# Optimization experiments

Hardware: AMD Instinct MI355X
Metric: run time of the kernel (lower is better)

## Reference

```python
import math
import jax, jax.numpy as jnp
import numpy as np

B, H, M, L, D, HID = 4, 8, 1024, 3200, 128, 1024
ATTN_LIM, RAMP = 2048, 128
PRE_DIV, LOSS_COEF = 16.0, 1e-06
SIZE = ATTN_LIM  # ExpireSpanDrop size = args.attn_lim


def skew(X, pad_value):
    # X: (BH, M, K) -> (BH, M, K+M), shifting row i right by i (relative-pos trick)
    BH, Mq, K = X.shape
    X = jnp.pad(X, ((0, 0), (0, 0), (0, Mq + 1)), constant_values=pad_value)
    X = X.reshape(BH, -1)[:, :-Mq]
    return X.reshape(BH, Mq, K + Mq)


def setup_inputs():
    key = jax.random.key(0)
    ks = jax.random.split(key, 6)
    query = jax.random.normal(ks[0], (B * H, M, D), jnp.float32)
    k = jax.random.normal(ks[1], (B * H, L, D), jnp.float32)
    v = jax.random.normal(ks[2], (B * H, L, D), jnp.float32)
    memory_hid = jax.random.normal(ks[3], (B, L, HID), jnp.float32)
    # age counters: oldest slot first; the current block (last M slots) goes down to -(M-1)
    memory_counter = jnp.broadcast_to(
        jnp.arange(L - 1, -1, -1, dtype=jnp.float32) - (M - 1), (B, L))
    key_pe = 0.02 * jax.random.normal(ks[4], (1, D, M), jnp.float32)
    span_w = 0.01 * jax.random.normal(ks[5], (1, HID), jnp.float32)
    span_b = jnp.full((1,), -math.log(1.0 / 0.1 - 1.0), jnp.float32)  # init_percentage=0.1
    return {"query": query, "key": k, "value": v, "memory_hid": memory_hid,
            "memory_counter": memory_counter, "key_pe": key_pe,
            "span_w": span_w, "span_b": span_b}


def reference(query, key, value, memory_hid, memory_counter, key_pe, span_w, span_b):
    max_mem = ATTN_LIM + M + RAMP
    # QK^T
    attn = jnp.einsum('bmd,bld->bml', query, key)                              # (BH, M, L)
    # --- ExpireSpanDrop (eval mode, no noise) ---
    max_span = jax.nn.sigmoid(
        jnp.einsum('blh,oh->blo', memory_hid / PRE_DIV, span_w)[..., 0] + span_b[0]) * SIZE  # (B, L)
    remaining_offset = max_span - memory_counter                               # (B, L)
    remaining_span = remaining_offset[:, None, :] - jnp.arange(M, dtype=jnp.float32)[None, :, None]  # (B, M, L)
    emask = jnp.clip(remaining_span / RAMP + 1.0, 0.0, 1.0)
    ramp_mask = ((emask > 0) & (emask < 1)).astype(emask.dtype)
    aux_loss = (remaining_span * ramp_mask).sum((-1, -2)) / RAMP / M * LOSS_COEF  # (B,)
    # causal mask (precomputed buffer in torch)
    causal = jnp.tril(jnp.ones((M, max_mem), jnp.float32), k=max_mem - M - 1)[:, -L:]
    mask = jnp.broadcast_to((emask * causal)[:, None], (B, H, M, L)).reshape(B * H, M, L)
    # --- relative position bias via skew ---
    attn_pos = skew(jnp.einsum('bmd,dk->bmk', query, key_pe[0]), 0.0)          # (BH, M, 2M)
    attn = attn.at[:, :, -2 * M:].add(attn_pos)
    # masked softmax + renormalization by soft mask
    attn = jnp.where(mask == 0, -jnp.inf, attn) / math.sqrt(D)
    attn = jax.nn.softmax(attn, axis=-1)
    attn = attn * mask
    attn = attn / (attn.sum(-1, keepdims=True) + 1e-08)
    out = jnp.einsum('bml,bld->bmd', attn, value)                              # (BH, M, D)
    return out, aux_loss, remaining_offset
```

## Files before the change

kernel.cpp:

```cpp
#include <hip/hip_runtime.h>
#include <stdint.h>

#define B_   4
#define H_   8
#define BH_  32
#define M_   1024
#define L_   3200
#define D_   128
#define HID_ 1024
#define NT64 50
#define CAUSAL_K 2175
#define POS_OFF  1152
#define SCALE 0.08838834764831845f
#define NEGV (-3.0e38f)
#define NEGH (-1.0e38f)

typedef short  bf16x8 __attribute__((ext_vector_type(8)));
typedef float  f32x4  __attribute__((ext_vector_type(4)));

__device__ __forceinline__ unsigned short f2bf(float x) {
    union { float f; uint32_t u; } v; v.f = x;
    return (unsigned short)((v.u + 0x7FFFu + ((v.u >> 16) & 1u)) >> 16);
}
__device__ __forceinline__ float bf2f(unsigned short h) {
    union { uint32_t u; float f; } v; v.u = ((uint32_t)h) << 16; return v.f;
}
__device__ __forceinline__ uint32_t pack_bf2(float lo, float hi) {
    union { float f; uint32_t u; } a, b; a.f = lo; b.f = hi;
    return __builtin_amdgcn_perm(b.u, a.u, 0x07060302u);
}

template <int CTRL>
__device__ __forceinline__ float dpp_movf(float x) {
    union { float f; int i; } u; u.f = x;
    u.i = __builtin_amdgcn_update_dpp(0, u.i, CTRL, 0xF, 0xF, true);
    return u.f;
}
__device__ __forceinline__ float row_max16(float x) {
    x = fmaxf(x, dpp_movf<0xB1>(x));
    x = fmaxf(x, dpp_movf<0x4E>(x));
    x = fmaxf(x, dpp_movf<0x141>(x));
    x = fmaxf(x, dpp_movf<0x140>(x));
    return x;
}
__device__ __forceinline__ float row_sum16(float x) {
    x += dpp_movf<0xB1>(x);
    x += dpp_movf<0x4E>(x);
    x += dpp_movf<0x141>(x);
    x += dpp_movf<0x140>(x);
    return x;
}

__global__ void span_kernel(const float* __restrict__ hid,
                            const float* __restrict__ counter,
                            const float* __restrict__ sw,
                            const float* __restrict__ sb,
                            float* __restrict__ r0_ws,
                            float* __restrict__ r0_out) {
    const int row  = blockIdx.x * 4 + (threadIdx.x >> 6);
    const int lane = threadIdx.x & 63;
    const float* h = hid + (size_t)row * HID_;
    float acc = 0.f;
#pragma unroll
    for (int it = 0; it < 4; ++it) {
        const int k = it * 256 + lane * 4;
        const float4 a = *(const float4*)(h + k);
        const float4 w = *(const float4*)(sw + k);
        acc += a.x*w.x + a.y*w.y + a.z*w.z + a.w*w.w;
    }
#pragma unroll
    for (int off = 32; off; off >>= 1) acc += __shfl_down(acc, off);
    if (lane == 0) {
        const float x  = acc * (1.0f/16.0f) + sb[0];
        const float ms = 2048.0f / (1.0f + __expf(-x));
        const float r0 = ms - counter[row];
        r0_ws[row]  = r0;
        r0_out[row] = r0;
    }
}

__global__ void tilemax_kernel(const float* __restrict__ r0_ws,
                               float* __restrict__ tmax) {
    const int t = blockIdx.x;
    const int lane = threadIdx.x;
    float v = r0_ws[t * 64 + lane];
#pragma unroll
    for (int off = 32; off; off >>= 1) v = fmaxf(v, __shfl_down(v, off));
    if (lane == 0) tmax[t] = v;
}

__global__ void aux_kernel(const float* __restrict__ r0_ws,
                           float* __restrict__ aux_out) {
    const int b = blockIdx.x, tid = threadIdx.x;
    float s = 0.f;
    for (int l = tid; l < L_; l += 256) {
        const float r = r0_ws[b * L_ + l];
        const int fl = (int)floorf(r);
        int mlo = fl + 1;   if (mlo < 0) mlo = 0;
        int mhi = fl + 128; if (mhi > M_ - 1) mhi = M_ - 1;
        const int n = mhi - mlo + 1;
        if (n > 0) s += (float)n * r - 0.5f * (float)(mlo + mhi) * (float)n;
    }
    __shared__ float red[256];
    red[tid] = s; __syncthreads();
    for (int st = 128; st; st >>= 1) {
        if (tid < st) red[tid] += red[tid + st];
        __syncthreads();
    }
    if (tid == 0) aux_out[b] = red[0] * (1.0f/128.0f) * (1.0f/1024.0f) * 1e-6f;
}

__global__ void pet_kernel(const float* __restrict__ PE,
                           unsigned short* __restrict__ PET) {
    const int tid = threadIdx.x;
    const int c = blockIdx.x * 4 + (tid >> 6);
    const int e = tid & 63;
    const float lo = PE[(2*e)   * M_ + c];
    const float hi = PE[(2*e+1) * M_ + c];
    ((uint32_t*)PET)[c * 64 + e] = pack_bf2(lo, hi);
}

#define KS_STR 136
#define VT_STR 72
#define PE_STR 136
#define P_STR  72
#define T_STR  72

__global__ void __launch_bounds__(256, 2)
attn_kernel(const float* __restrict__ Q, const float* __restrict__ K,
            const float* __restrict__ V, const unsigned short* __restrict__ PET,
            const float* __restrict__ r0g, const float* __restrict__ tmax,
            float* __restrict__ out) {
    __shared__ short Ks[64 * KS_STR];
    __shared__ short Vt[128 * VT_STR];
    __shared__ short PEs[64 * PE_STR];
    __shared__ short Tb[2][64 * T_STR];
    __shared__ short Pb[64 * P_STR];
    __shared__ float r0s[64];
    __shared__ float tfl[NT64];

    const int bh = blockIdx.y;
    const int b  = bh >> 3;
    const int i0 = blockIdx.x << 6;
    const int tid  = threadIdx.x;
    const int wave = tid >> 6;
    const int lane = tid & 63;
    const int lq   = lane & 15;
    const int quad = lane >> 4;
    const int lt_end = min(NT64, (int)blockIdx.x + 35);

    if (tid < NT64) tfl[tid] = tmax[b * NT64 + tid];
    __syncthreads();
    const float live_thresh = (float)(i0 - 128);

    auto next_live = [&](int s) {
        while (s < lt_end && !(tfl[s] > live_thresh)) ++s;
        return s;
    };

    float4 kp[8];
    float4 vpa[4], vpb[4];
    uint4  pep[4];
    float  r0p = 0.f;

    auto issue_prefetch = [&](int plt) {
        const int l0p = plt << 6;
        const float* kb = K + ((size_t)bh * L_ + l0p) * D_;
        const float* vb = V + ((size_t)bh * L_ + l0p) * D_;
#pragma unroll
        for (int it = 0; it < 8; ++it) {
            const int f = it * 256 + tid;
            kp[it] = *(const float4*)(kb + (f >> 5) * D_ + (f & 31) * 4);
        }
        const int p2 = (tid & 31) * 2;
#pragma unroll
        for (int it = 0; it < 4; ++it) {
            const int c = it * 8 + (tid >> 5);
            vpa[it] = *(const float4*)(vb + (size_t)p2 * D_ + c * 4);
            vpb[it] = *(const float4*)(vb + (size_t)(p2 + 1) * D_ + c * 4);
        }
        const int c0p = l0p - i0 - POS_OFF;
#pragma unroll
        for (int it = 0; it < 4; ++it) {
            const int f = it * 256 + tid;
            const int cg = c0p + (f >> 4);
            if ((unsigned)cg < (unsigned)M_)
                pep[it] = *(const uint4*)(PET + (size_t)cg * D_ + (f & 15) * 8);
            else { pep[it].x = 0; pep[it].y = 0; pep[it].z = 0; pep[it].w = 0; }
        }
        if (tid < 64) r0p = r0g[b * L_ + l0p + tid];
    };

    auto write_stage = [&]() {
#pragma unroll
        for (int it = 0; it < 8; ++it) {
            const int f = it * 256 + tid;
            uint2 w;
            w.x = pack_bf2(kp[it].x, kp[it].y);
            w.y = pack_bf2(kp[it].z, kp[it].w);
            *(uint2*)&Ks[(f >> 5) * KS_STR + (f & 31) * 4] = w;
        }
        const int p2 = (tid & 31) * 2;
#pragma unroll
        for (int it = 0; it < 4; ++it) {
            const int c = it * 8 + (tid >> 5);
            const float* a = (const float*)&vpa[it];
            const float* bb = (const float*)&vpb[it];
#pragma unroll
            for (int j = 0; j < 4; ++j)
                *(uint32_t*)&Vt[(c * 4 + j) * VT_STR + p2] = pack_bf2(a[j], bb[j]);
        }
#pragma unroll
        for (int it = 0; it < 4; ++it) {
            const int f = it * 256 + tid;
            *(uint4*)&PEs[(f >> 4) * PE_STR + (f & 15) * 8] = pep[it];
        }
        if (tid < 64) r0s[tid] = r0p;
    };

    int lt = next_live(0);
    if (lt < lt_end) issue_prefetch(lt);

    bf16x8 qfrag[4];
    {
        const float* qp = Q + ((size_t)bh * M_ + (i0 + wave * 16 + lq)) * D_;
#pragma unroll
        for (int kk = 0; kk < 4; ++kk) {
            const float4 q0 = *(const float4*)(qp + kk * 32 + quad * 8);
            const float4 q1 = *(const float4*)(qp + kk * 32 + quad * 8 + 4);
            union { bf16x8 v; uint32_t u[4]; } qq;
            qq.u[0] = pack_bf2(q0.x, q0.y); qq.u[1] = pack_bf2(q0.z, q0.w);
            qq.u[2] = pack_bf2(q1.x, q1.y); qq.u[3] = pack_bf2(q1.z, q1.w);
            qfrag[kk] = qq.v;
        }
    }

    auto computeT = [&](short* tb) {
#pragma unroll
        for (int nt = 0; nt < 4; ++nt) {
            f32x4 acc = (f32x4){0.f, 0.f, 0.f, 0.f};
#pragma unroll
            for (int kk = 0; kk < 4; ++kk) {
                const bf16x8 bf = *(const bf16x8*)&PEs[(nt*16 + lq) * PE_STR + kk*32 + quad*8];
                acc = __builtin_amdgcn_mfma_f32_16x16x32_bf16(qfrag[kk], bf, acc, 0, 0, 0);
            }
#pragma unroll
            for (int r = 0; r < 4; ++r) {
                union { float f; uint32_t u; } t; t.f = acc[r];
                tb[(wave*16 + quad*4 + r) * T_STR + nt*16 + lq] = (short)(t.u >> 16);
            }
        }
    };

    f32x4 oacc[8];
#pragma unroll
    for (int d = 0; d < 8; ++d) oacc[d] = (f32x4){0.f, 0.f, 0.f, 0.f};
    float mrun[4] = {NEGV, NEGV, NEGV, NEGV};
    float Zr[4]   = {0.f, 0.f, 0.f, 0.f};
    float Zm[4]   = {0.f, 0.f, 0.f, 0.f};
    int tlo = 0, thi = 1;
    int prev_c0 = -(1 << 30);

    while (lt < lt_end) {
        const int l0 = lt << 6;
        const int c0 = l0 - i0 - POS_OFF;
        const bool need_pos = (c0 + 63 >= 0) && (c0 - 63 <= M_ - 1);
        const bool rolling  = need_pos && (prev_c0 == c0 - 64);

        __syncthreads();
        write_stage();
        __syncthreads();

        const int ltn = next_live(lt + 1);
        if (ltn < lt_end) issue_prefetch(ltn);

        f32x4 sfrag[4];
#pragma unroll
        for (int nt = 0; nt < 4; ++nt) {
            f32x4 acc = (f32x4){0.f, 0.f, 0.f, 0.f};
#pragma unroll
            for (int kk = 0; kk < 4; ++kk) {
                const bf16x8 bf = *(const bf16x8*)&Ks[(nt*16 + lq) * KS_STR + kk*32 + quad*8];
                acc = __builtin_amdgcn_mfma_f32_16x16x32_bf16(qfrag[kk], bf, acc, 0, 0, 0);
            }
            sfrag[nt] = acc;
        }

        if (need_pos) {
            if (rolling) {
                const int t = tlo; tlo = thi; thi = t;
                computeT(&Tb[thi][0]);
            } else {
                tlo = 0; thi = 1;
                computeT(&Tb[1][0]);
                uint4 lowp[4];
#pragma unroll
                for (int it = 0; it < 4; ++it) {
                    const int f = it * 256 + tid;
                    const int cg = (c0 - 64) + (f >> 4);
                    if ((unsigned)cg < (unsigned)M_)
                        lowp[it] = *(const uint4*)(PET + (size_t)cg * D_ + (f & 15) * 8);
                    else { lowp[it].x = 0; lowp[it].y = 0; lowp[it].z = 0; lowp[it].w = 0; }
                }
                __syncthreads();
#pragma unroll
                for (int it = 0; it < 4; ++it) {
                    const int f = it * 256 + tid;
                    *(uint4*)&PEs[(f >> 4) * PE_STR + (f & 15) * 8] = lowp[it];
                }
                __syncthreads();
                computeT(&Tb[0][0]);
            }
            prev_c0 = c0;
        } else {
            prev_c0 = -(1 << 30);
        }

        float rv[4];
#pragma unroll
        for (int nt = 0; nt < 4; ++nt) rv[nt] = r0s[nt*16 + lq];

        float sv[4][4], em[4][4];
#pragma unroll
        for (int r = 0; r < 4; ++r) {
            const int iq = i0 + wave*16 + quad*4 + r;
            const float fiq = (float)iq;
#pragma unroll
            for (int nt = 0; nt < 4; ++nt) {
                const int l = l0 + nt*16 + lq;
                float s = sfrag[nt][r];
                const int c = l - iq - POS_OFF;
                if (need_pos && (unsigned)c < (unsigned)M_) {
                    const int cb = c - (c0 - 64);
                    const short* tbp = (cb & 64) ? &Tb[thi][0] : &Tb[tlo][0];
                    s += bf2f((unsigned short)tbp[(wave*16 + quad*4 + r) * T_STR + (cb & 63)]);
                }
                const float e = fminf(fmaxf((rv[nt] - fiq) * 0.0078125f + 1.0f, 0.f), 1.f);
                em[r][nt] = e;
                const bool live = (l <= iq + CAUSAL_K) && (e > 0.f);
                sv[r][nt] = live ? s * SCALE : NEGV;
            }
        }

#pragma unroll
        for (int r = 0; r < 4; ++r) {
            float v = fmaxf(fmaxf(sv[r][0], sv[r][1]), fmaxf(sv[r][2], sv[r][3]));
            v = row_max16(v);
            const float nm = fmaxf(mrun[r], v);
            float alpha = 1.f, psum = 0.f, pmsum = 0.f, pmv[4];
            if (nm > NEGH) {
                alpha = (mrun[r] > NEGH) ? __expf(mrun[r] - nm) : 0.f;
#pragma unroll
                for (int nt = 0; nt < 4; ++nt) {
                    const float p = __expf(sv[r][nt] - nm);
                    const float pm = p * em[r][nt];
                    psum += p; pmsum += pm; pmv[nt] = pm;
                }
            } else {
                pmv[0] = pmv[1] = pmv[2] = pmv[3] = 0.f;
            }
            psum  = row_sum16(psum);
            pmsum = row_sum16(pmsum);
            mrun[r] = nm;
            Zr[r] = Zr[r] * alpha + psum;
            Zm[r] = Zm[r] * alpha + pmsum;
#pragma unroll
            for (int d = 0; d < 8; ++d) oacc[d][r] *= alpha;
#pragma unroll
            for (int nt = 0; nt < 4; ++nt) {
                union { float f; uint32_t u; } t; t.f = pmv[nt];
                Pb[(wave*16 + quad*4 + r) * P_STR + nt*16 + lq] = (short)(t.u >> 16);
            }
        }

#pragma unroll
        for (int kk = 0; kk < 2; ++kk) {
            const bf16x8 pf = *(const bf16x8*)&Pb[(wave*16 + lq) * P_STR + kk*32 + quad*8];
#pragma unroll
            for (int dt = 0; dt < 8; ++dt) {
                const bf16x8 vf = *(const bf16x8*)&Vt[(dt*16 + lq) * VT_STR + kk*32 + quad*8];
                oacc[dt] = __builtin_amdgcn_mfma_f32_16x16x32_bf16(pf, vf, oacc[dt], 0, 0, 0);
            }
        }
        lt = ltn;
    }

#pragma unroll
    for (int r = 0; r < 4; ++r) {
        const int iq = i0 + wave*16 + quad*4 + r;
        const float inv = 1.0f / (Zm[r] + 1e-8f * Zr[r]);
        float* op = out + ((size_t)bh * M_ + iq) * D_;
#pragma unroll
        for (int dt = 0; dt < 8; ++dt)
            op[dt*16 + lq] = oacc[dt][r] * inv;
    }
}

__global__ void __launch_bounds__(256, 2)
attn_fb_kernel(const float* __restrict__ Q, const float* __restrict__ K,
               const float* __restrict__ V, const float* __restrict__ PE,
               const float* __restrict__ r0g, const float* __restrict__ tmax,
               float* __restrict__ out) {
    __shared__ short Ks[64 * KS_STR];
    __shared__ short Vt[128 * VT_STR];
    __shared__ short PEP[64 * PE_STR];
    __shared__ short Tb[2][64 * T_STR];
    __shared__ float r0s[64];

    const int bh = blockIdx.y;
    const int b  = bh >> 3;
    const int i0 = blockIdx.x << 6;
    const int tid  = threadIdx.x;
    const int wave = tid >> 6;
    const int lane = tid & 63;
    const int lq   = lane & 15;
    const int quad = lane >> 4;

    bf16x8 qfrag[4];
    {
        const float* qp = Q + ((size_t)bh * M_ + (i0 + wave * 16 + lq)) * D_;
#pragma unroll
        for (int kk = 0; kk < 4; ++kk) {
            const float* p = qp + kk * 32 + quad * 8;
            bf16x8 f;
#pragma unroll
            for (int j = 0; j < 8; ++j) f[j] = (short)f2bf(p[j]);
            qfrag[kk] = f;
        }
    }

    f32x4 oacc[8];
#pragma unroll
    for (int d = 0; d < 8; ++d) oacc[d] = (f32x4){0.f, 0.f, 0.f, 0.f};
    float mrun[4] = {NEGV, NEGV, NEGV, NEGV};
    float Zr[4]   = {0.f, 0.f, 0.f, 0.f};
    float Zm[4]   = {0.f, 0.f, 0.f, 0.f};

    int tlo = 0, thi = 1;
    int prev_c0 = -100000;

    auto stagePE = [&](int cbase) {
#pragma unroll
        for (int it = 0; it < 8; ++it) {
            const int f4 = it * 256 + tid;
            const int d  = f4 >> 4;
            const int cl = (f4 & 15) << 2;
#pragma unroll
            for (int j = 0; j < 4; ++j) {
                const int cg = cbase + cl + j;
                const float v = (cg >= 0 && cg < M_) ? PE[d * M_ + cg] : 0.f;
                PEP[(cl + j) * PE_STR + d] = (short)f2bf(v);
            }
        }
    };
    auto computeT = [&](short* tb) {
#pragma unroll
        for (int nt = 0; nt < 4; ++nt) {
            f32x4 acc = (f32x4){0.f, 0.f, 0.f, 0.f};
#pragma unroll
            for (int kk = 0; kk < 4; ++kk) {
                const bf16x8 bf = *(const bf16x8*)&PEP[(nt*16 + lq) * PE_STR + kk*32 + quad*8];
                acc = __builtin_amdgcn_mfma_f32_16x16x32_bf16(qfrag[kk], bf, acc, 0, 0, 0);
            }
#pragma unroll
            for (int r = 0; r < 4; ++r)
                tb[(wave*16 + quad*4 + r) * T_STR + nt*16 + lq] = (short)f2bf(acc[r]);
        }
    };

    const int lt_end = min(NT64, (int)blockIdx.x + 35);
    for (int lt = 0; lt < lt_end; ++lt) {
        const int l0 = lt << 6;
        if (!(tmax[b * NT64 + lt] > (float)(i0 - 128))) continue;

        __syncthreads();
        {
            const float* kbase = K + ((size_t)bh * L_ + l0) * D_;
            const float* vbase = V + ((size_t)bh * L_ + l0) * D_;
#pragma unroll
            for (int it = 0; it < 8; ++it) {
                const int f4 = it * 256 + tid;
                const int row = f4 >> 5;
                const int ds  = (f4 & 31) << 2;
                const float4 kv = *(const float4*)(kbase + row * D_ + ds);
                uint2 pk;
                pk.x = (uint32_t)f2bf(kv.x) | ((uint32_t)f2bf(kv.y) << 16);
                pk.y = (uint32_t)f2bf(kv.z) | ((uint32_t)f2bf(kv.w) << 16);
                *(uint2*)&Ks[row * KS_STR + ds] = pk;
                const float4 vv = *(const float4*)(vbase + row * D_ + ds);
                Vt[(ds+0) * VT_STR + row] = (short)f2bf(vv.x);
                Vt[(ds+1) * VT_STR + row] = (short)f2bf(vv.y);
                Vt[(ds+2) * VT_STR + row] = (short)f2bf(vv.z);
                Vt[(ds+3) * VT_STR + row] = (short)f2bf(vv.w);
            }
            if (tid < 64) r0s[tid] = r0g[b * L_ + l0 + tid];
        }

        const int c0 = l0 - i0 - POS_OFF;
        const bool need_pos = (c0 + 63 >= 0) && (c0 - 63 <= M_ - 1);
        if (need_pos) {
            if (prev_c0 == c0 - 64) {
                const int t = tlo; tlo = thi; thi = t;
                stagePE(c0);
                __syncthreads();
                computeT(&Tb[thi][0]);
            } else {
                stagePE(c0 - 64);
                __syncthreads();
                computeT(&Tb[0][0]);
                __syncthreads();
                stagePE(c0);
                __syncthreads();
                computeT(&Tb[1][0]);
                tlo = 0; thi = 1;
            }
            prev_c0 = c0;
        } else {
            __syncthreads();
        }

        f32x4 sfrag[4];
#pragma unroll
        for (int nt = 0; nt < 4; ++nt) {
            f32x4 acc = (f32x4){0.f, 0.f, 0.f, 0.f};
#pragma unroll
            for (int kk = 0; kk < 4; ++kk) {
                const bf16x8 bf = *(const bf16x8*)&Ks[(nt*16 + lq) * KS_STR + kk*32 + quad*8];
                acc = __builtin_amdgcn_mfma_f32_16x16x32_bf16(qfrag[kk], bf, acc, 0, 0, 0);
            }
            sfrag[nt] = acc;
        }
        __syncthreads();

        float sv[4][4];
#pragma unroll
        for (int r = 0; r < 4; ++r) {
            const int iq = i0 + wave*16 + quad*4 + r;
#pragma unroll
            for (int nt = 0; nt < 4; ++nt) {
                const int l = l0 + nt*16 + lq;
                float s = sfrag[nt][r];
                const int c = l - iq - POS_OFF;
                if (c >= 0 && c < M_) {
                    const int cb = c - (c0 - 64);
                    const short* tbp = (cb & 64) ? &Tb[thi][0] : &Tb[tlo][0];
                    s += bf2f((unsigned short)tbp[(wave*16 + quad*4 + r) * T_STR + (cb & 63)]);
                }
                const float e = fminf(fmaxf((r0s[nt*16 + lq] - (float)iq) * 0.0078125f + 1.0f, 0.f), 1.f);
                const bool live = (l <= iq + CAUSAL_K) && (e > 0.f);
                sv[r][nt] = live ? s * SCALE : NEGV;
            }
        }

#pragma unroll
        for (int r = 0; r < 4; ++r) {
            float v = fmaxf(fmaxf(sv[r][0], sv[r][1]), fmaxf(sv[r][2], sv[r][3]));
            v = row_max16(v);
            const float nm = fmaxf(mrun[r], v);
            float alpha, pmv[4];
            float psum = 0.f, pmsum = 0.f;
            if (nm > NEGH) {
                alpha = (mrun[r] > NEGH) ? __expf(mrun[r] - nm) : 0.f;
                const int iq = i0 + wave*16 + quad*4 + r;
#pragma unroll
                for (int nt = 0; nt < 4; ++nt) {
                    const float p = __expf(sv[r][nt] - nm);
                    const float e = fminf(fmaxf((r0s[nt*16 + lq] - (float)iq) * 0.0078125f + 1.0f, 0.f), 1.f);
                    const float pm = p * e;
                    psum += p; pmsum += pm; pmv[nt] = pm;
                }
            } else {
                alpha = 1.f;
                pmv[0] = pmv[1] = pmv[2] = pmv[3] = 0.f;
            }
            psum  = row_sum16(psum);
            pmsum = row_sum16(pmsum);
            mrun[r] = nm;
            Zr[r] = Zr[r] * alpha + psum;
            Zm[r] = Zm[r] * alpha + pmsum;
#pragma unroll
            for (int d = 0; d < 8; ++d) oacc[d][r] *= alpha;
#pragma unroll
            for (int nt = 0; nt < 4; ++nt)
                PEP[(wave*16 + quad*4 + r) * P_STR + nt*16 + lq] = (short)f2bf(pmv[nt]);
        }
        __syncthreads();

#pragma unroll
        for (int kk = 0; kk < 2; ++kk) {
            const bf16x8 pf = *(const bf16x8*)&PEP[(wave*16 + lq) * P_STR + kk*32 + quad*8];
#pragma unroll
            for (int dt = 0; dt < 8; ++dt) {
                const bf16x8 vf = *(const bf16x8*)&Vt[(dt*16 + lq) * VT_STR + kk*32 + quad*8];
                oacc[dt] = __builtin_amdgcn_mfma_f32_16x16x32_bf16(pf, vf, oacc[dt], 0, 0, 0);
            }
        }
    }

#pragma unroll
    for (int r = 0; r < 4; ++r) {
        const int iq = i0 + wave*16 + quad*4 + r;
        const float inv = 1.0f / (Zm[r] + 1e-8f * Zr[r]);
        float* op = out + ((size_t)bh * M_ + iq) * D_;
#pragma unroll
        for (int dt = 0; dt < 8; ++dt)
            op[dt*16 + lq] = oacc[dt][r] * inv;
    }
}

extern "C" void kernel_launch(void* const* d_in, const int* in_sizes, int n_in,
                              void* d_out, int out_size, void* d_ws, size_t ws_size,
                              hipStream_t stream) {
    (void)in_sizes; (void)n_in; (void)out_size;
    const float* Q       = (const float*)d_in[0];
    const float* K       = (const float*)d_in[1];
    const float* V       = (const float*)d_in[2];
    const float* hid     = (const float*)d_in[3];
    const float* counter = (const float*)d_in[4];
    const float* pe      = (const float*)d_in[5];
    const float* sw      = (const float*)d_in[6];
    const float* sb      = (const float*)d_in[7];

    float* out    = (float*)d_out;
    float* aux    = out + (size_t)BH_ * M_ * D_;
    float* r0_out = aux + B_;

    float* r0_ws = (float*)d_ws;
    float* tmax  = r0_ws + B_ * L_;
    unsigned short* PET = (unsigned short*)(r0_ws + 13056);
    const bool use_pet = ws_size >= (size_t)(13056 * 4 + M_ * D_ * 2);

    span_kernel<<<(B_ * L_) / 4, 256, 0, stream>>>(hid, counter, sw, sb, r0_ws, r0_out);
    tilemax_kernel<<<B_ * NT64, 64, 0, stream>>>(r0_ws, tmax);
    if (use_pet) {
        pet_kernel<<<M_ / 4, 256, 0, stream>>>(pe, PET);
        attn_kernel<<<dim3(M_ / 64, BH_), 256, 0, stream>>>(Q, K, V, PET, r0_ws, tmax, out);
    } else {
        attn_fb_kernel<<<dim3(M_ / 64, BH_), 256, 0, stream>>>(Q, K, V, pe, r0_ws, tmax, out);
    }
    aux_kernel<<<B_, 256, 0, stream>>>(r0_ws, aux);
}
```

Before: 237.0 us.

## Split attention key columns across 8 waves with shared-memory softmax merge

```diff
diff --git a/kernel.cpp b/kernel.cpp
--- a/kernel.cpp
+++ b/kernel.cpp
@@ -125,42 +125,51 @@
 #define PE_STR 136
 #define P_STR  72
 #define T_STR  72
-
-__global__ void __launch_bounds__(256, 2)
+#define SM_STR 12
+#define EP_STR 132
+
+
+__global__ void __launch_bounds__(512, 4)
 attn_kernel(const float* __restrict__ Q, const float* __restrict__ K,
             const float* __restrict__ V, const unsigned short* __restrict__ PET,
             const float* __restrict__ r0g, const float* __restrict__ tmax,
             float* __restrict__ out) {
-    __shared__ short Ks[64 * KS_STR];
-    __shared__ short Vt[128 * VT_STR];
-    __shared__ short PEs[64 * PE_STR];
-    __shared__ short Tb[2][64 * T_STR];
-    __shared__ short Pb[64 * P_STR];
-    __shared__ float r0s[64];
-    __shared__ float tfl[NT64];
+    __shared__ __align__(16) char SMEM[66816];
+    short* Ks  = (short*)SMEM;
+    short* Vt  = (short*)(SMEM + 17408);
+    short* Tb0 = (short*)(SMEM + 35840);
+    short* Tb1 = (short*)(SMEM + 45056);
+    short* Pb  = (short*)(SMEM + 54272);
+    float* r0s = (float*)(SMEM + 63488);
+    float* SMf = (float*)(SMEM + 63744);
+    float* EPf = (float*)SMEM;
 
     const int bh = blockIdx.y;
     const int b  = bh >> 3;
     const int i0 = blockIdx.x << 6;
     const int tid  = threadIdx.x;
     const int wave = tid >> 6;
+    const int wr   = wave & 3;
+    const int wc   = wave >> 2;
     const int lane = tid & 63;
     const int lq   = lane & 15;
     const int quad = lane >> 4;
     const int lt_end = min(NT64, (int)blockIdx.x + 35);
 
-    if (tid < NT64) tfl[tid] = tmax[b * NT64 + tid];
-    __syncthreads();
     const float live_thresh = (float)(i0 - 128);
-
-    auto next_live = [&](int s) {
-        while (s < lt_end && !(tfl[s] > live_thresh)) ++s;
-        return s;
+    unsigned long long live_mask;
+    {
+        const int sidx = (lane < NT64) ? lane : (NT64 - 1);
+        const float tv = tmax[b * NT64 + sidx];
+        live_mask = __ballot((lane < NT64) && (lane < lt_end) && (tv > live_thresh));
+    }
+    auto next_live = [&](int s) -> int {
+        const unsigned long long m = live_mask >> s;
+        return m ? (s + __builtin_ctzll(m)) : lt_end;
     };
 
-    float4 kp[8];
-    float4 vpa[4], vpb[4];
-    uint4  pep[4];
+    float4 kp[4];
+    float4 vpa[2], vpb[2];
     float  r0p = 0.f;
 
     auto issue_prefetch = [&](int plt) {
@@ -168,33 +177,24 @@
         const float* kb = K + ((size_t)bh * L_ + l0p) * D_;
         const float* vb = V + ((size_t)bh * L_ + l0p) * D_;
 #pragma unroll
-        for (int it = 0; it < 8; ++it) {
-            const int f = it * 256 + tid;
+        for (int it = 0; it < 4; ++it) {
+            const int f = it * 512 + tid;
             kp[it] = *(const float4*)(kb + (f >> 5) * D_ + (f & 31) * 4);
         }
         const int p2 = (tid & 31) * 2;
 #pragma unroll
-        for (int it = 0; it < 4; ++it) {
-            const int c = it * 8 + (tid >> 5);
+        for (int it = 0; it < 2; ++it) {
+            const int c = it * 16 + (tid >> 5);
             vpa[it] = *(const float4*)(vb + (size_t)p2 * D_ + c * 4);
             vpb[it] = *(const float4*)(vb + (size_t)(p2 + 1) * D_ + c * 4);
         }
-        const int c0p = l0p - i0 - POS_OFF;
-#pragma unroll
-        for (int it = 0; it < 4; ++it) {
-            const int f = it * 256 + tid;
-            const int cg = c0p + (f >> 4);
-            if ((unsigned)cg < (unsigned)M_)
-                pep[it] = *(const uint4*)(PET + (size_t)cg * D_ + (f & 15) * 8);
-            else { pep[it].x = 0; pep[it].y = 0; pep[it].z = 0; pep[it].w = 0; }
-        }
         if (tid < 64) r0p = r0g[b * L_ + l0p + tid];
     };
 
     auto write_stage = [&]() {
 #pragma unroll
-        for (int it = 0; it < 8; ++it) {
-            const int f = it * 256 + tid;
+        for (int it = 0; it < 4; ++it) {
+            const int f = it * 512 + tid;
             uint2 w;
             w.x = pack_bf2(kp[it].x, kp[it].y);
             w.y = pack_bf2(kp[it].z, kp[it].w);
@@ -202,19 +202,14 @@
         }
         const int p2 = (tid & 31) * 2;
 #pragma unroll
-        for (int it = 0; it < 4; ++it) {
-            const int c = it * 8 + (tid >> 5);
+        for (int it = 0; it < 2; ++it) {
+            const int c = it * 16 + (tid >> 5);
             const float* a = (const float*)&vpa[it];
             const float* bb = (const float*)&vpb[it];
 #pragma unroll
             for (int j = 0; j < 4; ++j)
                 *(uint32_t*)&Vt[(c * 4 + j) * VT_STR + p2] = pack_bf2(a[j], bb[j]);
         }
-#pragma unroll
-        for (int it = 0; it < 4; ++it) {
-            const int f = it * 256 + tid;
-            *(uint4*)&PEs[(f >> 4) * PE_STR + (f & 15) * 8] = pep[it];
-        }
         if (tid < 64) r0s[tid] = r0p;
     };
 
@@ -223,7 +218,7 @@
 
     bf16x8 qfrag[4];
     {
-        const float* qp = Q + ((size_t)bh * M_ + (i0 + wave * 16 + lq)) * D_;
+        const float* qp = Q + ((size_t)bh * M_ + (i0 + wr * 16 + lq)) * D_;
 #pragma unroll
         for (int kk = 0; kk < 4; ++kk) {
             const float4 q0 = *(const float4*)(qp + kk * 32 + quad * 8);
@@ -235,19 +230,22 @@
         }
     }
 
-    auto computeT = [&](short* tb) {
+    auto computeT_g = [&](int cbase, short* tb) {
 #pragma unroll
         for (int nt = 0; nt < 4; ++nt) {
+            int cg = cbase + nt * 16 + lq;
+            cg = min(max(cg, 0), M_ - 1);
+            const unsigned short* pp = PET + (size_t)cg * D_ + quad * 8;
             f32x4 acc = (f32x4){0.f, 0.f, 0.f, 0.f};
 #pragma unroll
             for (int kk = 0; kk < 4; ++kk) {
-                const bf16x8 bf = *(const bf16x8*)&PEs[(nt*16 + lq) * PE_STR + kk*32 + quad*8];
+                const bf16x8 bf = *(const bf16x8*)(pp + kk * 32);
                 acc = __builtin_amdgcn_mfma_f32_16x16x32_bf16(qfrag[kk], bf, acc, 0, 0, 0);
             }
 #pragma unroll
             for (int r = 0; r < 4; ++r) {
                 union { float f; uint32_t u; } t; t.f = acc[r];
-                tb[(wave*16 + quad*4 + r) * T_STR + nt*16 + lq] = (short)(t.u >> 16);
+                tb[(wr * 16 + quad * 4 + r) * T_STR + nt * 16 + lq] = (short)(t.u >> 16);
             }
         }
     };
@@ -274,125 +272,133 @@
         const int ltn = next_live(lt + 1);
         if (ltn < lt_end) issue_prefetch(ltn);
 
-        f32x4 sfrag[4];
-#pragma unroll
-        for (int nt = 0; nt < 4; ++nt) {
+        if (need_pos) {
+            if (rolling) {
+                const int t = tlo; tlo = thi; thi = t;
+                computeT_g(c0, thi ? Tb1 : Tb0);
+            } else {
+                tlo = 0; thi = 1;
+                computeT_g(c0 - 64, Tb0);
+                computeT_g(c0, Tb1);
+            }
+            prev_c0 = c0;
+        } else {
+            prev_c0 = -(1 << 30);
+        }
+
+        f32x4 sfrag[2];
+#pragma unroll
+        for (int nt2 = 0; nt2 < 2; ++nt2) {
+            const int nt = wc * 2 + nt2;
             f32x4 acc = (f32x4){0.f, 0.f, 0.f, 0.f};
 #pragma unroll
             for (int kk = 0; kk < 4; ++kk) {
                 const bf16x8 bf = *(const bf16x8*)&Ks[(nt*16 + lq) * KS_STR + kk*32 + quad*8];
                 acc = __builtin_amdgcn_mfma_f32_16x16x32_bf16(qfrag[kk], bf, acc, 0, 0, 0);
             }
-            sfrag[nt] = acc;
-        }
-
-        if (need_pos) {
-            if (rolling) {
-                const int t = tlo; tlo = thi; thi = t;
-                computeT(&Tb[thi][0]);
-            } else {
-                tlo = 0; thi = 1;
-                computeT(&Tb[1][0]);
-                uint4 lowp[4];
-#pragma unroll
-                for (int it = 0; it < 4; ++it) {
-                    const int f = it * 256 + tid;
-                    const int cg = (c0 - 64) + (f >> 4);
-                    if ((unsigned)cg < (unsigned)M_)
-                        lowp[it] = *(const uint4*)(PET + (size_t)cg * D_ + (f & 15) * 8);
-                    else { lowp[it].x = 0; lowp[it].y = 0; lowp[it].z = 0; lowp[it].w = 0; }
-                }
-                __syncthreads();
-#pragma unroll
-                for (int it = 0; it < 4; ++it) {
-                    const int f = it * 256 + tid;
-                    *(uint4*)&PEs[(f >> 4) * PE_STR + (f & 15) * 8] = lowp[it];
-                }
-                __syncthreads();
-                computeT(&Tb[0][0]);
-            }
-            prev_c0 = c0;
-        } else {
-            prev_c0 = -(1 << 30);
-        }
-
-        float rv[4];
-#pragma unroll
-        for (int nt = 0; nt < 4; ++nt) rv[nt] = r0s[nt*16 + lq];
-
-        float sv[4][4], em[4][4];
+            sfrag[nt2] = acc;
+        }
+
+        float rv[2];
+        rv[0] = r0s[(wc*2 + 0) * 16 + lq];
+        rv[1] = r0s[(wc*2 + 1) * 16 + lq];
+
+        float pmv[4][2];
 #pragma unroll
         for (int r = 0; r < 4; ++r) {
-            const int iq = i0 + wave*16 + quad*4 + r;
+            const int iq = i0 + wr*16 + quad*4 + r;
             const float fiq = (float)iq;
-#pragma unroll
-            for (int nt = 0; nt < 4; ++nt) {
+            float sv[2];
+#pragma unroll
+            for (int nt2 = 0; nt2 < 2; ++nt2) {
+                const int nt = wc*2 + nt2;
                 const int l = l0 + nt*16 + lq;
-                float s = sfrag[nt][r];
+                float s = sfrag[nt2][r];
                 const int c = l - iq - POS_OFF;
                 if (need_pos && (unsigned)c < (unsigned)M_) {
                     const int cb = c - (c0 - 64);
-                    const short* tbp = (cb & 64) ? &Tb[thi][0] : &Tb[tlo][0];
-                    s += bf2f((unsigned short)tbp[(wave*16 + quad*4 + r) * T_STR + (cb & 63)]);
+                    const short* tbp = (cb & 64) ? (thi ? Tb1 : Tb0) : (tlo ? Tb1 : Tb0);
+                    s += bf2f((unsigned short)tbp[(wr*16 + quad*4 + r) * T_STR + (cb & 63)]);
                 }
-                const float e = fminf(fmaxf((rv[nt] - fiq) * 0.0078125f + 1.0f, 0.f), 1.f);
-                em[r][nt] = e;
+                const float e = fminf(fmaxf((rv[nt2] - fiq) * 0.0078125f + 1.0f, 0.f), 1.f);
                 const bool live = (l <= iq + CAUSAL_K) && (e > 0.f);
-                sv[r][nt] = live ? s * SCALE : NEGV;
-            }
-        }
+                sv[nt2] = live ? s * SCALE : NEGV;
+            }
+            float lm = fmaxf(sv[0], sv[1]);
+            lm = row_max16(lm);
+            const float p0 = __expf(sv[0] - lm);
+            const float p1 = __expf(sv[1] - lm);
+            const float e0 = fminf(fmaxf((rv[0] - fiq) * 0.0078125f + 1.0f, 0.f), 1.f);
+            const float e1 = fminf(fmaxf((rv[1] - fiq) * 0.0078125f + 1.0f, 0.f), 1.f);
+            const float pm0 = p0 * e0, pm1 = p1 * e1;
+            const float psum  = row_sum16(p0 + p1);
+            const float pmsum = row_sum16(pm0 + pm1);
+            pmv[r][0] = pm0; pmv[r][1] = pm1;
+            if (lq == 0) {
+                float4 st; st.x = lm; st.y = psum; st.z = pmsum; st.w = 0.f;
+                *(float4*)&SMf[(wr*16 + quad*4 + r) * SM_STR + wc*4] = st;
+            }
+        }
+        __syncthreads();
 
 #pragma unroll
         for (int r = 0; r < 4; ++r) {
-            float v = fmaxf(fmaxf(sv[r][0], sv[r][1]), fmaxf(sv[r][2], sv[r][3]));
-            v = row_max16(v);
-            const float nm = fmaxf(mrun[r], v);
-            float alpha = 1.f, psum = 0.f, pmsum = 0.f, pmv[4];
+            const int row = wr*16 + quad*4 + r;
+            const float4 s0 = *(const float4*)&SMf[row * SM_STR + 0];
+            const float4 s1 = *(const float4*)&SMf[row * SM_STR + 4];
+            const float nm = fmaxf(mrun[r], fmaxf(s0.x, s1.x));
             if (nm > NEGH) {
-                alpha = (mrun[r] > NEGH) ? __expf(mrun[r] - nm) : 0.f;
-#pragma unroll
-                for (int nt = 0; nt < 4; ++nt) {
-                    const float p = __expf(sv[r][nt] - nm);
-                    const float pm = p * em[r][nt];
-                    psum += p; pmsum += pm; pmv[nt] = pm;
-                }
+                const float alpha = __expf(mrun[r] - nm);
+                const float cf0   = __expf(s0.x - nm);
+                const float cf1   = __expf(s1.x - nm);
+                Zr[r] = Zr[r] * alpha + s0.y * cf0 + s1.y * cf1;
+                Zm[r] = Zm[r] * alpha + s0.z * cf0 + s1.z * cf1;
+                mrun[r] = nm;
+                const float cw = wc ? cf1 : cf0;
+#pragma unroll
+                for (int d = 0; d < 8; ++d) oacc[d][r] *= alpha;
+                pmv[r][0] *= cw; pmv[r][1] *= cw;
             } else {
-                pmv[0] = pmv[1] = pmv[2] = pmv[3] = 0.f;
-            }
-            psum  = row_sum16(psum);
-            pmsum = row_sum16(pmsum);
-            mrun[r] = nm;
-            Zr[r] = Zr[r] * alpha + psum;
-            Zm[r] = Zm[r] * alpha + pmsum;
-#pragma unroll
-            for (int d = 0; d < 8; ++d) oacc[d][r] *= alpha;
-#pragma unroll
-            for (int nt = 0; nt < 4; ++nt) {
-                union { float f; uint32_t u; } t; t.f = pmv[nt];
-                Pb[(wave*16 + quad*4 + r) * P_STR + nt*16 + lq] = (short)(t.u >> 16);
-            }
-        }
-
-#pragma unroll
-        for (int kk = 0; kk < 2; ++kk) {
-            const bf16x8 pf = *(const bf16x8*)&Pb[(wave*16 + lq) * P_STR + kk*32 + quad*8];
+                pmv[r][0] = 0.f; pmv[r][1] = 0.f;
+            }
+            union { float f; uint32_t u; } t0, t1;
+            t0.f = pmv[r][0]; t1.f = pmv[r][1];
+            Pb[row * P_STR + (wc*2 + 0)*16 + lq] = (short)(t0.u >> 16);
+            Pb[row * P_STR + (wc*2 + 1)*16 + lq] = (short)(t1.u >> 16);
+        }
+
+        {
+            const bf16x8 pf = *(const bf16x8*)&Pb[(wr*16 + lq) * P_STR + wc*32 + quad*8];
 #pragma unroll
             for (int dt = 0; dt < 8; ++dt) {
-                const bf16x8 vf = *(const bf16x8*)&Vt[(dt*16 + lq) * VT_STR + kk*32 + quad*8];
+                const bf16x8 vf = *(const bf16x8*)&Vt[(dt*16 + lq) * VT_STR + wc*32 + quad*8];
                 oacc[dt] = __builtin_amdgcn_mfma_f32_16x16x32_bf16(pf, vf, oacc[dt], 0, 0, 0);
             }
         }
         lt = ltn;
     }
 
-#pragma unroll
-    for (int r = 0; r < 4; ++r) {
-        const int iq = i0 + wave*16 + quad*4 + r;
-        const float inv = 1.0f / (Zm[r] + 1e-8f * Zr[r]);
-        float* op = out + ((size_t)bh * M_ + iq) * D_;
+    __syncthreads();
+    if (wc == 1) {
 #pragma unroll
         for (int dt = 0; dt < 8; ++dt)
-            op[dt*16 + lq] = oacc[dt][r] * inv;
+#pragma unroll
+            for (int r = 0; r < 4; ++r)
+                EPf[(wr*16 + quad*4 + r) * EP_STR + dt*16 + lq] = oacc[dt][r];
+    }
+    __syncthreads();
+    if (wc == 0) {
+#pragma unroll
+        for (int r = 0; r < 4; ++r) {
+            const int iq = i0 + wr*16 + quad*4 + r;
+            const float inv = 1.0f / (Zm[r] + 1e-8f * Zr[r]);
+            float* op = out + ((size_t)bh * M_ + iq) * D_;
+#pragma unroll
+            for (int dt = 0; dt < 8; ++dt) {
+                const float v = oacc[dt][r] + EPf[(wr*16 + quad*4 + r) * EP_STR + dt*16 + lq];
+                op[dt*16 + lq] = v * inv;
+            }
+        }
     }
 }
 
@@ -634,7 +640,7 @@
     tilemax_kernel<<<B_ * NT64, 64, 0, stream>>>(r0_ws, tmax);
     if (use_pet) {
         pet_kernel<<<M_ / 4, 256, 0, stream>>>(pe, PET);
-        attn_kernel<<<dim3(M_ / 64, BH_), 256, 0, stream>>>(Q, K, V, PET, r0_ws, tmax, out);
+        attn_kernel<<<dim3(M_ / 64, BH_), 512, 0, stream>>>(Q, K, V, PET, r0_ws, tmax, out);
     } else {
         attn_fb_kernel<<<dim3(M_ / 64, BH_), 256, 0, stream>>>(Q, K, V, pe, r0_ws, tmax, out);
     }
```

Measured after the change: 327.6 us. +38.3%, slower.

## Cut attention LDS footprint for higher occupancy and fuse prep kernels

Applied to the files above, without the earlier changes.

```diff
diff --git a/kernel.cpp b/kernel.cpp
--- a/kernel.cpp
+++ b/kernel.cpp
@@ -51,14 +51,17 @@
     return x;
 }
 
-__global__ void span_kernel(const float* __restrict__ hid,
-                            const float* __restrict__ counter,
-                            const float* __restrict__ sw,
-                            const float* __restrict__ sb,
-                            float* __restrict__ r0_ws,
-                            float* __restrict__ r0_out) {
-    const int row  = blockIdx.x * 4 + (threadIdx.x >> 6);
-    const int lane = threadIdx.x & 63;
+__global__ void span_pet_kernel(const float* __restrict__ hid,
+                                const float* __restrict__ counter,
+                                const float* __restrict__ sw,
+                                const float* __restrict__ sb,
+                                const float* __restrict__ PE,
+                                float* __restrict__ r0_ws,
+                                float* __restrict__ r0_out,
+                                unsigned short* __restrict__ PET) {
+    const int tid  = threadIdx.x;
+    const int row  = blockIdx.x * 4 + (tid >> 6);
+    const int lane = tid & 63;
     const float* h = hid + (size_t)row * HID_;
     float acc = 0.f;
 #pragma unroll
@@ -77,67 +80,63 @@
         r0_ws[row]  = r0;
         r0_out[row] = r0;
     }
-}
-
-__global__ void tilemax_kernel(const float* __restrict__ r0_ws,
-                               float* __restrict__ tmax) {
-    const int t = blockIdx.x;
-    const int lane = threadIdx.x;
-    float v = r0_ws[t * 64 + lane];
-#pragma unroll
-    for (int off = 32; off; off >>= 1) v = fmaxf(v, __shfl_down(v, off));
-    if (lane == 0) tmax[t] = v;
-}
-
-__global__ void aux_kernel(const float* __restrict__ r0_ws,
-                           float* __restrict__ aux_out) {
-    const int b = blockIdx.x, tid = threadIdx.x;
-    float s = 0.f;
-    for (int l = tid; l < L_; l += 256) {
-        const float r = r0_ws[b * L_ + l];
-        const int fl = (int)floorf(r);
-        int mlo = fl + 1;   if (mlo < 0) mlo = 0;
-        int mhi = fl + 128; if (mhi > M_ - 1) mhi = M_ - 1;
-        const int n = mhi - mlo + 1;
-        if (n > 0) s += (float)n * r - 0.5f * (float)(mlo + mhi) * (float)n;
-    }
+    if (PET != nullptr && blockIdx.x < M_ / 4) {
+        const int c = blockIdx.x * 4 + (tid >> 6);
+        const int e = tid & 63;
+        const float lo = PE[(2*e)   * M_ + c];
+        const float hi = PE[(2*e+1) * M_ + c];
+        ((uint32_t*)PET)[c * 64 + e] = pack_bf2(lo, hi);
+    }
+}
+
+__global__ void prep_kernel(const float* __restrict__ r0_ws,
+                            float* __restrict__ tmax,
+                            float* __restrict__ aux_out) {
     __shared__ float red[256];
-    red[tid] = s; __syncthreads();
-    for (int st = 128; st; st >>= 1) {
-        if (tid < st) red[tid] += red[tid + st];
-        __syncthreads();
-    }
-    if (tid == 0) aux_out[b] = red[0] * (1.0f/128.0f) * (1.0f/1024.0f) * 1e-6f;
-}
-
-__global__ void pet_kernel(const float* __restrict__ PE,
-                           unsigned short* __restrict__ PET) {
+    const int bid = blockIdx.x;
     const int tid = threadIdx.x;
-    const int c = blockIdx.x * 4 + (tid >> 6);
-    const int e = tid & 63;
-    const float lo = PE[(2*e)   * M_ + c];
-    const float hi = PE[(2*e+1) * M_ + c];
-    ((uint32_t*)PET)[c * 64 + e] = pack_bf2(lo, hi);
+    if (bid < 50) {
+        const int wave = tid >> 6, lane = tid & 63;
+        const int t = bid * 4 + wave;
+        float v = r0_ws[t * 64 + lane];
+#pragma unroll
+        for (int off = 32; off; off >>= 1) v = fmaxf(v, __shfl_down(v, off));
+        if (lane == 0) tmax[t] = v;
+    } else {
+        const int b = bid - 50;
+        float s = 0.f;
+        for (int l = tid; l < L_; l += 256) {
+            const float r = r0_ws[b * L_ + l];
+            const int fl = (int)floorf(r);
+            int mlo = fl + 1;   if (mlo < 0) mlo = 0;
+            int mhi = fl + 128; if (mhi > M_ - 1) mhi = M_ - 1;
+            const int n = mhi - mlo + 1;
+            if (n > 0) s += (float)n * r - 0.5f * (float)(mlo + mhi) * (float)n;
+        }
+        red[tid] = s; __syncthreads();
+        for (int st = 128; st; st >>= 1) {
+            if (tid < st) red[tid] += red[tid + st];
+            __syncthreads();
+        }
+        if (tid == 0) aux_out[b] = red[0] * (1.0f/128.0f) * (1.0f/1024.0f) * 1e-6f;
+    }
 }
 
 #define KS_STR 136
 #define VT_STR 72
-#define PE_STR 136
-#define P_STR  72
 #define T_STR  72
 
-__global__ void __launch_bounds__(256, 2)
+
+__global__ void __launch_bounds__(256, 4)
 attn_kernel(const float* __restrict__ Q, const float* __restrict__ K,
             const float* __restrict__ V, const unsigned short* __restrict__ PET,
             const float* __restrict__ r0g, const float* __restrict__ tmax,
             float* __restrict__ out) {
-    __shared__ short Ks[64 * KS_STR];
-    __shared__ short Vt[128 * VT_STR];
-    __shared__ short PEs[64 * PE_STR];
-    __shared__ short Tb[2][64 * T_STR];
-    __shared__ short Pb[64 * P_STR];
-    __shared__ float r0s[64];
-    __shared__ float tfl[NT64];
+    __shared__ __align__(16) char SMEM[54272];
+    short* Ks  = (short*)SMEM;
+    short* Vt  = (short*)(SMEM + 17408);
+    short* Tb0 = (short*)(SMEM + 35840);
+    short* Tb1 = (short*)(SMEM + 45056);
 
     const int bh = blockIdx.y;
     const int b  = bh >> 3;
@@ -149,19 +148,22 @@
     const int quad = lane >> 4;
     const int lt_end = min(NT64, (int)blockIdx.x + 35);
 
-    if (tid < NT64) tfl[tid] = tmax[b * NT64 + tid];
-    __syncthreads();
     const float live_thresh = (float)(i0 - 128);
-
-    auto next_live = [&](int s) {
-        while (s < lt_end && !(tfl[s] > live_thresh)) ++s;
-        return s;
+    unsigned long long live_mask;
+    {
+        const int sidx = (lane < NT64) ? lane : (NT64 - 1);
+        const float tv = tmax[b * NT64 + sidx];
+        live_mask = __ballot((lane < NT64) && (lane < lt_end) && (tv > live_thresh));
+    }
+    auto next_live = [&](int s) -> int {
+        const unsigned long long m = live_mask >> s;
+        return m ? (s + __builtin_ctzll(m)) : lt_end;
     };
 
     float4 kp[8];
     float4 vpa[4], vpb[4];
-    uint4  pep[4];
-    float  r0p = 0.f;
+    float  rvp[4];
+    float  rv[4];
 
     auto issue_prefetch = [&](int plt) {
         const int l0p = plt << 6;
@@ -179,16 +181,9 @@
             vpa[it] = *(const float4*)(vb + (size_t)p2 * D_ + c * 4);
             vpb[it] = *(const float4*)(vb + (size_t)(p2 + 1) * D_ + c * 4);
         }
-        const int c0p = l0p - i0 - POS_OFF;
-#pragma unroll
-        for (int it = 0; it < 4; ++it) {
-            const int f = it * 256 + tid;
-            const int cg = c0p + (f >> 4);
-            if ((unsigned)cg < (unsigned)M_)
-                pep[it] = *(const uint4*)(PET + (size_t)cg * D_ + (f & 15) * 8);
-            else { pep[it].x = 0; pep[it].y = 0; pep[it].z = 0; pep[it].w = 0; }
-        }
-        if (tid < 64) r0p = r0g[b * L_ + l0p + tid];
+        const float* rb = r0g + b * L_ + l0p;
+#pragma unroll
+        for (int nt = 0; nt < 4; ++nt) rvp[nt] = rb[nt * 16 + lq];
     };
 
     auto write_stage = [&]() {
@@ -211,11 +206,7 @@
                 *(uint32_t*)&Vt[(c * 4 + j) * VT_STR + p2] = pack_bf2(a[j], bb[j]);
         }
 #pragma unroll
-        for (int it = 0; it < 4; ++it) {
-            const int f = it * 256 + tid;
-            *(uint4*)&PEs[(f >> 4) * PE_STR + (f & 15) * 8] = pep[it];
-        }
-        if (tid < 64) r0s[tid] = r0p;
+        for (int nt = 0; nt < 4; ++nt) rv[nt] = rvp[nt];
     };
 
     int lt = next_live(0);
@@ -235,19 +226,22 @@
         }
     }
 
-    auto computeT = [&](short* tb) {
+    auto computeT_g = [&](int cbase, short* tb) {
 #pragma unroll
         for (int nt = 0; nt < 4; ++nt) {
+            int cg = cbase + nt * 16 + lq;
+            cg = min(max(cg, 0), M_ - 1);
+            const unsigned short* pp = PET + (size_t)cg * D_ + quad * 8;
             f32x4 acc = (f32x4){0.f, 0.f, 0.f, 0.f};
 #pragma unroll
             for (int kk = 0; kk < 4; ++kk) {
-                const bf16x8 bf = *(const bf16x8*)&PEs[(nt*16 + lq) * PE_STR + kk*32 + quad*8];
+                const bf16x8 bf = *(const bf16x8*)(pp + kk * 32);
                 acc = __builtin_amdgcn_mfma_f32_16x16x32_bf16(qfrag[kk], bf, acc, 0, 0, 0);
             }
 #pragma unroll
             for (int r = 0; r < 4; ++r) {
                 union { float f; uint32_t u; } t; t.f = acc[r];
-                tb[(wave*16 + quad*4 + r) * T_STR + nt*16 + lq] = (short)(t.u >> 16);
+                tb[(wave * 16 + quad * 4 + r) * T_STR + nt * 16 + lq] = (short)(t.u >> 16);
             }
         }
     };
@@ -274,6 +268,21 @@
         const int ltn = next_live(lt + 1);
         if (ltn < lt_end) issue_prefetch(ltn);
 
+        if (need_pos) {
+            if (rolling) {
+                const int t = tlo; tlo = thi; thi = t;
+                computeT_g(c0, thi ? Tb1 : Tb0);
+            } else {
+                tlo = 0; thi = 1;
+                computeT_g(c0 - 64, Tb0);
+                computeT_g(c0, Tb1);
+            }
+            prev_c0 = c0;
+        } else {
+            prev_c0 = -(1 << 30);
+        }
+        short* PbCur = need_pos ? (tlo ? Tb1 : Tb0) : Tb0;
+
         f32x4 sfrag[4];
 #pragma unroll
         for (int nt = 0; nt < 4; ++nt) {
@@ -285,40 +294,6 @@
             }
             sfrag[nt] = acc;
         }
-
-        if (need_pos) {
-            if (rolling) {
-                const int t = tlo; tlo = thi; thi = t;
-                computeT(&Tb[thi][0]);
-            } else {
-                tlo = 0; thi = 1;
-                computeT(&Tb[1][0]);
-                uint4 lowp[4];
-#pragma unroll
-                for (int it = 0; it < 4; ++it) {
-                    const int f = it * 256 + tid;
-                    const int cg = (c0 - 64) + (f >> 4);
-                    if ((unsigned)cg < (unsigned)M_)
-                        lowp[it] = *(const uint4*)(PET + (size_t)cg * D_ + (f & 15) * 8);
-                    else { lowp[it].x = 0; lowp[it].y = 0; lowp[it].z = 0; lowp[it].w = 0; }
-                }
-                __syncthreads();
-#pragma unroll
-                for (int it = 0; it < 4; ++it) {
-                    const int f = it * 256 + tid;
-                    *(uint4*)&PEs[(f >> 4) * PE_STR + (f & 15) * 8] = lowp[it];
-                }
-                __syncthreads();
-                computeT(&Tb[0][0]);
-            }
-            prev_c0 = c0;
-        } else {
-            prev_c0 = -(1 << 30);
-        }
-
-        float rv[4];
-#pragma unroll
-        for (int nt = 0; nt < 4; ++nt) rv[nt] = r0s[nt*16 + lq];
 
         float sv[4][4], em[4][4];
 #pragma unroll
@@ -332,7 +307,7 @@
                 const int c = l - iq - POS_OFF;
                 if (need_pos && (unsigned)c < (unsigned)M_) {
                     const int cb = c - (c0 - 64);
-                    const short* tbp = (cb & 64) ? &Tb[thi][0] : &Tb[tlo][0];
+                    const short* tbp = (cb & 64) ? (thi ? Tb1 : Tb0) : (tlo ? Tb1 : Tb0);
                     s += bf2f((unsigned short)tbp[(wave*16 + quad*4 + r) * T_STR + (cb & 63)]);
                 }
                 const float e = fminf(fmaxf((rv[nt] - fiq) * 0.0078125f + 1.0f, 0.f), 1.f);
@@ -369,13 +344,13 @@
 #pragma unroll
             for (int nt = 0; nt < 4; ++nt) {
                 union { float f; uint32_t u; } t; t.f = pmv[nt];
-                Pb[(wave*16 + quad*4 + r) * P_STR + nt*16 + lq] = (short)(t.u >> 16);
+                PbCur[(wave*16 + quad*4 + r) * T_STR + nt*16 + lq] = (short)(t.u >> 16);
             }
         }
 
 #pragma unroll
         for (int kk = 0; kk < 2; ++kk) {
-            const bf16x8 pf = *(const bf16x8*)&Pb[(wave*16 + lq) * P_STR + kk*32 + quad*8];
+            const bf16x8 pf = *(const bf16x8*)&PbCur[(wave*16 + lq) * T_STR + kk*32 + quad*8];
 #pragma unroll
             for (int dt = 0; dt < 8; ++dt) {
                 const bf16x8 vf = *(const bf16x8*)&Vt[(dt*16 + lq) * VT_STR + kk*32 + quad*8];
@@ -395,6 +370,9 @@
             op[dt*16 + lq] = oacc[dt][r] * inv;
     }
 }
+
+#define PE_STR 136
+#define P_STR  72
 
 __global__ void __launch_bounds__(256, 2)
 attn_fb_kernel(const float* __restrict__ Q, const float* __restrict__ K,
@@ -630,13 +608,12 @@
     unsigned short* PET = (unsigned short*)(r0_ws + 13056);
     const bool use_pet = ws_size >= (size_t)(13056 * 4 + M_ * D_ * 2);
 
-    span_kernel<<<(B_ * L_) / 4, 256, 0, stream>>>(hid, counter, sw, sb, r0_ws, r0_out);
-    tilemax_kernel<<<B_ * NT64, 64, 0, stream>>>(r0_ws, tmax);
+    span_pet_kernel<<<(B_ * L_) / 4, 256, 0, stream>>>(
+        hid, counter, sw, sb, pe, r0_ws, r0_out, use_pet ? PET : nullptr);
+    prep_kernel<<<54, 256, 0, stream>>>(r0_ws, tmax, aux);
     if (use_pet) {
-        pet_kernel<<<M_ / 4, 256, 0, stream>>>(pe, PET);
         attn_kernel<<<dim3(M_ / 64, BH_), 256, 0, stream>>>(Q, K, V, PET, r0_ws, tmax, out);
     } else {
         attn_fb_kernel<<<dim3(M_ / 64, BH_), 256, 0, stream>>>(Q, K, V, pe, r0_ws, tmax, out);
     }
-    aux_kernel<<<B_, 256, 0, stream>>>(r0_ws, aux);
-}
+}
```

Measured after the change: 284.5 us. 20.0% more time.
